# Optimization experiments

Hardware: AMD Instinct MI355X
Metric: run time of the kernel (lower is better)

Reference implementation:

```python
import math
import jax, jax.numpy as jnp
import numpy as np

# dims: layers, batch, seq, hidden, heads, ffn-mult
L, B, S, D, H, FFN = 2, 4, 2048, 256, 8, 4
HD = D // H          # head dim (= head v dim, double_v_dim=False)
EPS = 1e-5
SCALE_BASE = 512


def _ln(x, w, b):
    mu = x.mean(-1, keepdims=True)
    var = x.var(-1, keepdims=True)
    return (x - mu) * jax.lax.rsqrt(var + EPS) * w + b


def _xpos_tables():
    half = HD // 2
    sv = (np.arange(0, HD, 2) + 0.4 * HD) / (1.4 * HD)            # [half]
    pos = np.arange(S, dtype=np.float64)
    scale = sv[None, :] ** (pos[:, None] / SCALE_BASE)            # [S, half]
    inv_freq = 1.0 / (10000.0 ** (np.arange(half) / half))
    ang = pos[:, None] * inv_freq[None, :]                        # [S, half]
    return (jnp.asarray(np.sin(ang), jnp.float32),
            jnp.asarray(np.cos(ang), jnp.float32),
            jnp.asarray(scale, jnp.float32))

SIN, COS, XSCALE = _xpos_tables()


def _xpos(x, downscale=False):
    # x: [B, H, S, HD]
    sc = 1.0 / XSCALE if downscale else XSCALE
    sin2 = jnp.repeat(SIN * sc, 2, axis=-1)                       # [S, HD]
    cos2 = jnp.repeat(COS * sc, 2, axis=-1)
    x1, x2 = x[..., 0::2], x[..., 1::2]
    xr = jnp.stack((-x2, x1), axis=-1).reshape(x.shape)           # rotate_every_two
    return x * cos2 + xr * sin2


def _decay_mask():
    g = 1.0 - jnp.exp(jnp.linspace(math.log(1 / 32), math.log(1 / 512), H))
    n = jnp.arange(S)[:, None]
    m = jnp.arange(S)[None, :]
    keep = n >= m
    expo = jnp.where(keep, n - m, 0).astype(jnp.float32)
    return jnp.where(keep, g[:, None, None] ** expo[None], 0.0)   # [H, S, S]

DMASK = _decay_mask()


def setup_inputs() -> dict:
    key = jax.random.key(0)
    ks = jax.random.split(key, 16)
    sc = 1.0 / D
    f32 = jnp.float32
    return {
        "X":     jax.random.normal(ks[0], (B, S, D), f32),
        "Wq":    jax.random.normal(ks[1], (L, D, D), f32) * sc,
        "Wk":    jax.random.normal(ks[2], (L, D, D), f32) * sc,
        "Wv":    jax.random.normal(ks[3], (L, D, D), f32) * sc,
        "Wg":    jax.random.normal(ks[4], (L, D, D), f32) * sc,
        "Wo":    jax.random.normal(ks[5], (L, D, D), f32) * sc,
        "gn_w":  jnp.ones((L, D), f32) + 0.02 * jax.random.normal(ks[6], (L, D), f32),
        "gn_b":  0.02 * jax.random.normal(ks[7], (L, D), f32),
        "ln1_w": jnp.ones((L, D), f32),
        "ln1_b": jnp.zeros((L, D), f32),
        "ln2_w": jnp.ones((L, D), f32),
        "ln2_b": jnp.zeros((L, D), f32),
        "w1":    jax.random.normal(ks[8], (L, D, FFN * D), f32) * 0.02,
        "b1":    0.02 * jax.random.normal(ks[9], (L, FFN * D), f32),
        "w2":    jax.random.normal(ks[10], (L, FFN * D, D), f32) * 0.02,
        "b2":    0.02 * jax.random.normal(ks[11], (L, D), f32),
        "lnf_w": jnp.ones((D,), f32),
        "lnf_b": jnp.zeros((D,), f32),
    }


def reference(X, Wq, Wk, Wv, Wg, Wo, gn_w, gn_b, ln1_w, ln1_b,
              ln2_w, ln2_b, w1, b1, w2, b2, lnf_w, lnf_b):
    x = X
    for i in range(L):
        xn = _ln(x, ln1_w[i], ln1_b[i])                           # [B,S,D]
        q = (xn @ Wq[i]).reshape(B, S, H, HD).transpose(0, 2, 1, 3)
        k = (xn @ Wk[i]).reshape(B, S, H, HD).transpose(0, 2, 1, 3)
        v = (xn @ Wv[i]).reshape(B, S, H, HD).transpose(0, 2, 1, 3)
        q = _xpos(q)
        k = _xpos(k, downscale=True)
        att = jnp.einsum('bhnd,bhmd->bhnm', q, k) * DMASK          # [B,H,S,S]
        y = jnp.einsum('bhnm,bhmd->bhnd', att, v)                  # [B,H,S,HD]
        # GroupNorm(heads, v_dim): per-(b, position, head) normalization
        mu = y.mean(-1, keepdims=True)
        var = y.var(-1, keepdims=True)
        y = (y - mu) * jax.lax.rsqrt(var + EPS)
        y = y.transpose(0, 2, 1, 3).reshape(B, S, D)               # concat heads
        y = y * gn_w[i] + gn_b[i]
        g = xn @ Wg[i]
        ret = (g * jax.nn.sigmoid(g) * y) @ Wo[i]                  # swish gate + out proj
        yres = ret + x
        yn = _ln(yres, ln2_w[i], ln2_b[i])
        f = jax.nn.gelu(yn @ w1[i] + b1[i], approximate=False) @ w2[i] + b2[i]
        x = _ln(f + yres, lnf_w, lnf_b)
    return x
```

## Files before the change

kernel.cpp:

```cpp
#include <hip/hip_runtime.h>
#include <hip/hip_bf16.h>

typedef __hip_bfloat16 bf16;
typedef unsigned short ushort_t;
typedef __attribute__((ext_vector_type(8))) short short8v;
typedef __attribute__((ext_vector_type(4))) float f32x4;
typedef __attribute__((ext_vector_type(4))) unsigned int uint4v;

#define LYR 2
#define BB 4
#define SS 2048
#define DD 256
#define HH 8
#define HDD 32
#define FFD 1024
#define MM (BB*SS)

__device__ __forceinline__ unsigned int cvtpk(float lo, float hi) {
  unsigned int r;
  asm("v_cvt_pk_bf16_f32 %0, %1, %2" : "=v"(r) : "v"(lo), "v"(hi));
  return r;
}
__device__ __forceinline__ ushort_t f2b1(float x) { return (ushort_t)cvtpk(x, x); }

__device__ __forceinline__ void gload_lds16(const void* g, void* l) {
  __builtin_amdgcn_global_load_lds((const __attribute__((address_space(1))) void*)g,
                                   (__attribute__((address_space(3))) void*)l, 16, 0, 0);
}

__device__ __forceinline__ float l2g_of(int h) {
  return log2f(1.0f - expf(-3.4657359028f - 0.3960841187f * (float)h));
}

struct WDesc { const float* src; bf16* dst; int K; int N; };
struct WDescA { WDesc d[14]; float* tsn; float* tcs; float* tsc; };
__global__ __launch_bounds__(256) void wconv_k(WDescA da) {
  if (blockIdx.z == 14) {
    int i = (blockIdx.y * 32 + blockIdx.x) * 256 + threadIdx.y * 32 + threadIdx.x;
    if (i >= SS * 16) return;
    int s = i >> 4, j = i & 15;
    float sv = (2.0f * (float)j + 0.4f * (float)HDD) / (1.4f * (float)HDD);
    da.tsc[i] = powf(sv, (float)s * (1.0f / 512.0f));
    float inv_freq = powf(10000.0f, -(float)j * (1.0f / 16.0f));
    float ang = (float)s * inv_freq;
    da.tsn[i] = sinf(ang);
    da.tcs[i] = cosf(ang);
    return;
  }
  WDesc dd = da.d[blockIdx.z];
  int n0 = blockIdx.x * 32, k0 = blockIdx.y * 32;
  if (n0 >= dd.N || k0 >= dd.K) return;
  __shared__ float t[32][33];
  int tx = threadIdx.x, ty = threadIdx.y;
  #pragma unroll
  for (int i = 0; i < 32; i += 8) t[ty + i][tx] = dd.src[(size_t)(k0 + ty + i) * dd.N + n0 + tx];
  __syncthreads();
  #pragma unroll
  for (int i = 0; i < 32; i += 8) dd.dst[(size_t)(n0 + ty + i) * dd.K + k0 + tx] = __float2bfloat16(t[tx][ty + i]);
}

template<typename OT>
__global__ __launch_bounds__(256) void ln_k(const float* __restrict__ in, const float* __restrict__ w,
    const float* __restrict__ b, OT* __restrict__ out)
{
  int row = blockIdx.x, t = threadIdx.x;
  float v = in[(size_t)row * DD + t];
  __shared__ float red[4];
  float s = v;
  #pragma unroll
  for (int m = 32; m >= 1; m >>= 1) s += __shfl_xor(s, m);
  if ((t & 63) == 0) red[t >> 6] = s;
  __syncthreads();
  float mu = (red[0] + red[1] + red[2] + red[3]) * (1.0f / 256.0f);
  float d = v - mu;
  float s2 = d * d;
  #pragma unroll
  for (int m = 32; m >= 1; m >>= 1) s2 += __shfl_xor(s2, m);
  __syncthreads();
  if ((t & 63) == 0) red[t >> 6] = s2;
  __syncthreads();
  float var = (red[0] + red[1] + red[2] + red[3]) * (1.0f / 256.0f);
  float o = d * rsqrtf(var + 1e-5f) * w[t] + b[t];
  if constexpr (sizeof(OT) == 2) out[(size_t)row * DD + t] = __float2bfloat16(o);
  else                           out[(size_t)row * DD + t] = o;
}

#define STAGEG(buf, k0s) { \
    _Pragma("unroll") \
    for (int i = 0; i < BM / 32; ++i) { \
      int slot = i * 256 + tid; int row = slot >> 3, blk = slot & 7; \
      gload_lds16(Au + (size_t)(bm + row) * K + (k0s) + ((blk ^ (row & 7))) * 8, &Al[buf][slot * 8]); \
    } \
    _Pragma("unroll") \
    for (int i = 0; i < BN / 32; ++i) { \
      int slot = i * 256 + tid; int row = slot >> 3, blk = slot & 7; \
      gload_lds16(Bu + (size_t)(bn + row) * K + (k0s) + ((blk ^ (row & 7))) * 8, &Bl[buf][slot * 8]); \
    } }

enum { E_QKVG = 0 };

template<int BM, int BN, int K, int EPI>
__global__ __launch_bounds__(256) void mgemm_k(const bf16* __restrict__ Ag, const bf16* __restrict__ Wt,
    void* o0, void* o1, void* o2, void* o3,
    const float* __restrict__ tsn, const float* __restrict__ tcs, const float* __restrict__ tsc)
{
  constexpr int MT = BM / 32, NT = BN / 32;
  constexpr int WMH = BM / 2, WNH = BN / 2;
  __shared__ __align__(16) ushort_t Al[2][BM * 64];
  __shared__ __align__(16) ushort_t Bl[2][BN * 64];
  const int bm = blockIdx.x * BM;
  const int bn = blockIdx.y * BN;
  const int tid = threadIdx.x;
  const int lane = tid & 63, w = tid >> 6;
  const int lg = lane >> 4, ln = lane & 15;
  const int wr = w >> 1, wc = w & 1;
  const ushort_t* Au = (const ushort_t*)Ag;
  const ushort_t* Bu = (const ushort_t*)Wt;
  f32x4 acc[MT][NT] = {};

  STAGEG(0, 0)
  asm volatile("s_waitcnt vmcnt(0)" ::: "memory");
  __builtin_amdgcn_s_barrier();

  int cur = 0;
  for (int k0 = 0; k0 < K; k0 += 64) {
    if (k0 + 64 < K) STAGEG(cur ^ 1, k0 + 64)
    #pragma unroll
    for (int kh = 0; kh < 2; ++kh) {
      short8v af[MT], bfr[NT];
      #pragma unroll
      for (int mt = 0; mt < MT; ++mt) {
        int row = wr * WMH + mt * 16 + ln;
        af[mt] = *(const short8v*)&Al[cur][row * 64 + (((kh * 4 + lg) ^ (row & 7))) * 8];
      }
      #pragma unroll
      for (int nt = 0; nt < NT; ++nt) {
        int row = wc * WNH + nt * 16 + ln;
        bfr[nt] = *(const short8v*)&Bl[cur][row * 64 + (((kh * 4 + lg) ^ (row & 7))) * 8];
      }
      #pragma unroll
      for (int mt = 0; mt < MT; ++mt)
        #pragma unroll
        for (int nt = 0; nt < NT; ++nt)
          acc[mt][nt] = __builtin_amdgcn_mfma_f32_16x16x32_bf16(af[mt], bfr[nt], acc[mt][nt], 0, 0, 0);
    }
    asm volatile("s_waitcnt vmcnt(0)" ::: "memory");
    __builtin_amdgcn_s_barrier();
    cur ^= 1;
  }

  #pragma unroll
  for (int mt = 0; mt < MT; ++mt)
    #pragma unroll
    for (int nt = 0; nt < NT; ++nt) {
      const int colbase = bn + wc * WNH + nt * 16;
      const int sec = colbase >> 8;
      const int c = (colbase & 255) + ln;
      const int grow0 = bm + wr * WMH + mt * 16 + lg * 4;
      if (sec <= 1) {
        const int jj = (c & 31) >> 1;
        const float l2g = l2g_of(c >> 5);
        #pragma unroll
        for (int r = 0; r < 4; ++r) {
          const int grow = grow0 + r;
          const int s = grow & (SS - 1);
          float v = acc[mt][nt][r];
          float pv = __shfl_xor(v, 1);
          float scv = tsc[s * 16 + jj];
          if (sec == 1) scv = 1.0f / scv;
          float ce = tcs[s * 16 + jj] * scv, se = tsn[s * 16 + jj] * scv;
          float o = (ln & 1) ? (v * ce + pv * se) : (v * ce - pv * se);
          if (sec == 0) o *= exp2f(l2g * (float)s);
          bf16* dst = (sec == 0) ? (bf16*)o0 : (bf16*)o1;
          dst[(size_t)grow * DD + c] = __float2bfloat16(o);
        }
      } else if (sec == 2) {
        const int b = grow0 >> 11, s0 = grow0 & (SS - 1);
        const int h = c >> 5, d = c & 31;
        const float nl2g = -l2g_of(h);
        float v0 = acc[mt][nt][0] * exp2f(nl2g * (float)(s0 + 0));
        float v1 = acc[mt][nt][1] * exp2f(nl2g * (float)(s0 + 1));
        float v2 = acc[mt][nt][2] * exp2f(nl2g * (float)(s0 + 2));
        float v3 = acc[mt][nt][3] * exp2f(nl2g * (float)(s0 + 3));
        uint2 pk;
        pk.x = cvtpk(v0, v1);
        pk.y = cvtpk(v2, v3);
        *(uint2*)((ushort_t*)o2 + ((size_t)(b * 8 + h) * 32 + d) * SS + s0) = pk;
      } else {
        #pragma unroll
        for (int r = 0; r < 4; ++r)
          ((float*)o3)[(size_t)(grow0 + r) * DD + c] = acc[mt][nt][r];
      }
    }
}

template<bool LAST>
__global__ __launch_bounds__(256) void ffn_mega(
    const bf16* __restrict__ ubg, const bf16* __restrict__ wotg,
    const bf16* __restrict__ w1tg, const bf16* __restrict__ w2tg,
    const float* __restrict__ b1v, const float* __restrict__ b2v,
    const float* __restrict__ resin,
    float* __restrict__ yres, bf16* __restrict__ xn, float* __restrict__ dout,
    const float* __restrict__ l2w, const float* __restrict__ l2b,
    const float* __restrict__ lfw, const float* __restrict__ lfb,
    const float* __restrict__ l1w, const float* __restrict__ l1b)
{
  __shared__ __align__(16) ushort_t Bs[2][256 * 64];
  __shared__ __align__(16) ushort_t AX[4096];
  __shared__ __align__(16) ushort_t Us[4096];

  const int bm = blockIdx.x * 16;
  const int tid = threadIdx.x;
  const int lane = tid & 63, w = tid >> 6;
  const int lg = lane >> 4, ln = lane & 15;
  const int row0 = lg * 4;
  const ushort_t* ubu  = (const ushort_t*)ubg;
  const ushort_t* wotu = (const ushort_t*)wotg;
  const ushort_t* w1tu = (const ushort_t*)w1tg;
  const ushort_t* w2tu = (const ushort_t*)w2tg;
  float* red = (float*)Us;

  float resv[4][4];
  #pragma unroll
  for (int nt = 0; nt < 4; ++nt) {
    const int gcol = w * 64 + nt * 16 + ln;
    #pragma unroll
    for (int r = 0; r < 4; ++r)
      resv[nt][r] = resin[(size_t)(bm + row0 + r) * DD + gcol];
  }

  #define STAGEB(buf, base, stride, koff) { \
    _Pragma("unroll") \
    for (int i = 0; i < 8; ++i) { \
      int slot = i * 256 + tid; int row = slot >> 3, blk = slot & 7; \
      gload_lds16((base) + (size_t)row * (stride) + (koff) + ((blk ^ (row & 7))) * 8, &Bs[buf][slot * 8]); \
    } }
  #define STAGEA(buf, koff) { \
    if (tid < 128) { int row = tid >> 3, blk = tid & 7; \
      gload_lds16(ubu + (size_t)(bm + row) * DD + (koff) + ((blk ^ (row & 7))) * 8, &AX[(buf) * 1024 + tid * 8]); } }
  #define DRAIN asm volatile("s_waitcnt vmcnt(0)" ::: "memory"); __builtin_amdgcn_s_barrier();

  STAGEA(0, 0)
  STAGEB(0, wotu, 256, 0)
  DRAIN
  int cur = 0;

  f32x4 accw[4] = {};
  #pragma unroll
  for (int s = 0; s < 4; ++s) {
    if (s < 3) { STAGEA(cur ^ 1, (s + 1) * 64) STAGEB(cur ^ 1, wotu, 256, (s + 1) * 64) }
    else       { STAGEB(cur ^ 1, w1tu, 256, 0) }
    #pragma unroll
    for (int kh = 0; kh < 2; ++kh) {
      short8v af = *(const short8v*)&AX[cur * 1024 + ln * 64 + (((kh * 4 + lg) ^ (ln & 7))) * 8];
      #pragma unroll
      for (int nt = 0; nt < 4; ++nt) {
        int row = w * 64 + nt * 16 + ln;
        short8v bf_ = *(const short8v*)&Bs[cur][row * 64 + (((kh * 4 + lg) ^ (row & 7))) * 8];
        accw[nt] = __builtin_amdgcn_mfma_f32_16x16x32_bf16(af, bf_, accw[nt], 0, 0, 0);
      }
    }
    DRAIN
    cur ^= 1;
  }

  float v[4][4];
  #pragma unroll
  for (int nt = 0; nt < 4; ++nt)
    #pragma unroll
    for (int r = 0; r < 4; ++r) v[nt][r] = accw[nt][r] + resv[nt][r];
  float mu[4], rsg[4];
  {
    #pragma unroll
    for (int r = 0; r < 4; ++r) {
      float s1 = 0.f, s2 = 0.f;
      #pragma unroll
      for (int nt = 0; nt < 4; ++nt) { s1 += v[nt][r]; s2 += v[nt][r] * v[nt][r]; }
      #pragma unroll
      for (int m = 8; m >= 1; m >>= 1) { s1 += __shfl_xor(s1, m); s2 += __shfl_xor(s2, m); }
      if (ln == 0) { red[(w * 16 + row0 + r) * 2] = s1; red[(w * 16 + row0 + r) * 2 + 1] = s2; }
    }
    __syncthreads();
    #pragma unroll
    for (int r = 0; r < 4; ++r) {
      float S = 0.f, S2 = 0.f;
      #pragma unroll
      for (int ww = 0; ww < 4; ++ww) { S += red[(ww * 16 + row0 + r) * 2]; S2 += red[(ww * 16 + row0 + r) * 2 + 1]; }
      float m_ = S * (1.0f / 256.0f);
      mu[r] = m_; rsg[r] = rsqrtf(S2 * (1.0f / 256.0f) - m_ * m_ + 1e-5f);
    }
  }
  __syncthreads();
  #pragma unroll
  for (int nt = 0; nt < 4; ++nt) {
    const int gcol = w * 64 + nt * 16 + ln;
    const float lwv = l2w[gcol], lbv = l2b[gcol];
    const int off = nt * 16 + ln, blk = off >> 3, sub = off & 7;
    #pragma unroll
    for (int r = 0; r < 4; ++r) {
      const int row = row0 + r;
      float xv = (v[nt][r] - mu[r]) * rsg[r] * lwv + lbv;
      AX[row * 256 + w * 64 + ((blk ^ (row & 7)) << 3) + sub] = f2b1(xv);
    }
  }
  __syncthreads();

  f32x4 acc2[4] = {};
  #pragma unroll
  for (int c = 0; c < 4; ++c) {
    f32x4 acc1[4] = {};
    #pragma unroll
    for (int s = 0; s < 4; ++s) {
      if (s < 3) { STAGEB(cur ^ 1, w1tu + (size_t)c * 65536, 256, (s + 1) * 64) }
      else       { STAGEB(cur ^ 1, w2tu + c * 256, 1024, 0) }
      #pragma unroll
      for (int kh = 0; kh < 2; ++kh) {
        short8v af = *(const short8v*)&AX[ln * 256 + s * 64 + (((kh * 4 + lg) ^ (ln & 7))) * 8];
        #pragma unroll
        for (int nt = 0; nt < 4; ++nt) {
          int row = w * 64 + nt * 16 + ln;
          short8v bf_ = *(const short8v*)&Bs[cur][row * 64 + (((kh * 4 + lg) ^ (row & 7))) * 8];
          acc1[nt] = __builtin_amdgcn_mfma_f32_16x16x32_bf16(af, bf_, acc1[nt], 0, 0, 0);
        }
      }
      DRAIN
      cur ^= 1;
    }
    #pragma unroll
    for (int nt = 0; nt < 4; ++nt) {
      const int gcol1 = c * 256 + w * 64 + nt * 16 + ln;
      const float bb = b1v[gcol1];
      const int off = nt * 16 + ln, blk = off >> 3, sub = off & 7;
      #pragma unroll
      for (int r = 0; r < 4; ++r) {
        const int row = row0 + r;
        float t = acc1[nt][r] + bb;
        t = 0.5f * t * (1.0f + erff(t * 0.70710678118654752f));
        Us[row * 256 + w * 64 + ((blk ^ (row & 7)) << 3) + sub] = f2b1(t);
      }
    }
    __syncthreads();
    #pragma unroll
    for (int s = 0; s < 4; ++s) {
      if (s < 3)      { STAGEB(cur ^ 1, w2tu + c * 256, 1024, (s + 1) * 64) }
      else if (c < 3) { STAGEB(cur ^ 1, w1tu + (size_t)(c + 1) * 65536, 256, 0) }
      #pragma unroll
      for (int kh = 0; kh < 2; ++kh) {
        short8v af = *(const short8v*)&Us[ln * 256 + s * 64 + (((kh * 4 + lg) ^ (ln & 7))) * 8];
        #pragma unroll
        for (int nt = 0; nt < 4; ++nt) {
          int row = w * 64 + nt * 16 + ln;
          short8v bf_ = *(const short8v*)&Bs[cur][row * 64 + (((kh * 4 + lg) ^ (row & 7))) * 8];
          acc2[nt] = __builtin_amdgcn_mfma_f32_16x16x32_bf16(af, bf_, acc2[nt], 0, 0, 0);
        }
      }
      DRAIN
      cur ^= 1;
    }
  }

  float f[4][4];
  #pragma unroll
  for (int nt = 0; nt < 4; ++nt) {
    const int gcol = w * 64 + nt * 16 + ln;
    const float bb = b2v[gcol];
    #pragma unroll
    for (int r = 0; r < 4; ++r) f[nt][r] = acc2[nt][r] + bb + v[nt][r];
  }
  {
    #pragma unroll
    for (int r = 0; r < 4; ++r) {
      float s1 = 0.f, s2 = 0.f;
      #pragma unroll
      for (int nt = 0; nt < 4; ++nt) { s1 += f[nt][r]; s2 += f[nt][r] * f[nt][r]; }
      #pragma unroll
      for (int m = 8; m >= 1; m >>= 1) { s1 += __shfl_xor(s1, m); s2 += __shfl_xor(s2, m); }
      if (ln == 0) { red[(w * 16 + row0 + r) * 2] = s1; red[(w * 16 + row0 + r) * 2 + 1] = s2; }
    }
    __syncthreads();
    #pragma unroll
    for (int r = 0; r < 4; ++r) {
      float S = 0.f, S2 = 0.f;
      #pragma unroll
      for (int ww = 0; ww < 4; ++ww) { S += red[(ww * 16 + row0 + r) * 2]; S2 += red[(ww * 16 + row0 + r) * 2 + 1]; }
      float m_ = S * (1.0f / 256.0f);
      mu[r] = m_; rsg[r] = rsqrtf(S2 * (1.0f / 256.0f) - m_ * m_ + 1e-5f);
    }
  }
  float u[4][4];
  #pragma unroll
  for (int nt = 0; nt < 4; ++nt) {
    const int gcol = w * 64 + nt * 16 + ln;
    const float lwv = lfw[gcol], lbv = lfb[gcol];
    #pragma unroll
    for (int r = 0; r < 4; ++r)
      u[nt][r] = (f[nt][r] - mu[r]) * rsg[r] * lwv + lbv;
  }
  if constexpr (LAST) {
    #pragma unroll
    for (int nt = 0; nt < 4; ++nt) {
      const int gcol = w * 64 + nt * 16 + ln;
      #pragma unroll
      for (int r = 0; r < 4; ++r)
        dout[(size_t)(bm + row0 + r) * DD + gcol] = u[nt][r];
    }
  } else {
    __syncthreads();
    #pragma unroll
    for (int r = 0; r < 4; ++r) {
      float s1 = 0.f, s2 = 0.f;
      #pragma unroll
      for (int nt = 0; nt < 4; ++nt) { s1 += u[nt][r]; s2 += u[nt][r] * u[nt][r]; }
      #pragma unroll
      for (int m = 8; m >= 1; m >>= 1) { s1 += __shfl_xor(s1, m); s2 += __shfl_xor(s2, m); }
      if (ln == 0) { red[(w * 16 + row0 + r) * 2] = s1; red[(w * 16 + row0 + r) * 2 + 1] = s2; }
    }
    __syncthreads();
    float mu2[4], rs2[4];
    #pragma unroll
    for (int r = 0; r < 4; ++r) {
      float S = 0.f, S2 = 0.f;
      #pragma unroll
      for (int ww = 0; ww < 4; ++ww) { S += red[(ww * 16 + row0 + r) * 2]; S2 += red[(ww * 16 + row0 + r) * 2 + 1]; }
      float m_ = S * (1.0f / 256.0f);
      mu2[r] = m_; rs2[r] = rsqrtf(S2 * (1.0f / 256.0f) - m_ * m_ + 1e-5f);
    }
    #pragma unroll
    for (int nt = 0; nt < 4; ++nt) {
      const int gcol = w * 64 + nt * 16 + ln;
      const float lwv = l1w[gcol], lbv = l1b[gcol];
      #pragma unroll
      for (int r = 0; r < 4; ++r) {
        const size_t idx = (size_t)(bm + row0 + r) * DD + gcol;
        yres[idx] = u[nt][r];
        xn[idx] = __float2bfloat16((u[nt][r] - mu2[r]) * rs2[r] * lwv + lbv);
      }
    }
  }
  #undef STAGEB
  #undef STAGEA
  #undef DRAIN
}

__global__ __launch_bounds__(256) void attn_k(const bf16* __restrict__ qg, const bf16* __restrict__ kg,
    const bf16* __restrict__ vtg, const float* __restrict__ gbuf,
    const float* __restrict__ gnw, const float* __restrict__ gnb, bf16* __restrict__ ub)
{
  __shared__ __align__(16) ushort_t Kl[2][64 * 32];
  __shared__ __align__(16) ushort_t Vl[2][32 * 64];
  __shared__ __align__(16) unsigned int Pl[4][512];

  const int bh = blockIdx.x;
  const int b = bh >> 3, h = bh & (HH - 1);
  const int n0 = ((int)gridDim.y - 1 - (int)blockIdx.y) * 64;
  const int tid = threadIdx.x;
  const int w = tid >> 6, lane = tid & 63;
  const int lg = lane >> 4, ln = lane & 15;

  const size_t base = (size_t)b * SS * DD + h * HDD;
  const ushort_t* qp = (const ushort_t*)qg + base;
  const ushort_t* kp = (const ushort_t*)kg + base;
  const ushort_t* vtp = (const ushort_t*)vtg + (size_t)(b * 8 + h) * 32 * SS;

  const int n = n0 + w * 16 + ln;
  const short8v qf = *(const short8v*)(qp + (size_t)n * DD + lg * 8);

  const float l2g = l2g_of(h);
  f32x4 acc0 = {0,0,0,0}, acc1 = {0,0,0,0};

  const int Wwin = (int)(20.0f / (-l2g)) + 1;
  int m_lo = 0;
  if (n0 > Wwin) m_lo = ((n0 - Wwin) >> 6) << 6;

  const int Krow = tid >> 2, Kc8 = tid & 3;
  const int Vrow = tid >> 3, Vc8 = tid & 7;

  #define STAGE(buf, m0s) { \
    gload_lds16(kp + (size_t)((m0s) + Krow) * DD + ((Kc8 ^ (Krow & 3)) * 8), &Kl[buf][tid * 8]); \
    gload_lds16(vtp + (size_t)Vrow * SS + (m0s) + ((Vc8 ^ (Vrow & 7)) * 8), &Vl[buf][tid * 8]); }

  STAGE(0, m_lo)
  asm volatile("s_waitcnt vmcnt(0)" ::: "memory");
  __builtin_amdgcn_s_barrier();

  int cur = 0;
  for (int m0 = m_lo; m0 <= n0; m0 += 64) {
    if (m0 < n0) STAGE(cur ^ 1, m0 + 64)
    const bool diag = (m0 == n0);
    __builtin_amdgcn_s_setprio(1);
    #pragma unroll
    for (int mt = 0; mt < 4; ++mt) {
      const int krow = mt * 16 + ln;
      short8v kf = *(const short8v*)&Kl[cur][krow * 32 + ((lg ^ (krow & 3)) << 3)];
      f32x4 z = {0,0,0,0};
      f32x4 pa = __builtin_amdgcn_mfma_f32_16x16x32_bf16(kf, qf, z, 0, 0, 0);
      float v0 = pa[0], v1 = pa[1], v2 = pa[2], v3 = pa[3];
      if (diag) {
        const int m = n0 + mt * 16 + lg * 4;
        v0 = (n < m)     ? 0.f : v0;
        v1 = (n < m + 1) ? 0.f : v1;
        v2 = (n < m + 2) ? 0.f : v2;
        v3 = (n < m + 3) ? 0.f : v3;
      }
      uint2 pk;
      pk.x = cvtpk(v0, v1);
      pk.y = cvtpk(v2, v3);
      const int blk = (mt * 2 + (lg >> 1)) ^ (ln & 7);
      *(uint2*)&Pl[w][ln * 32 + blk * 4 + (lg & 1) * 2] = pk;
    }
    #pragma unroll
    for (int hh = 0; hh < 2; ++hh) {
      const int pblk = (hh * 4 + lg) ^ (ln & 7);
      uint4v pw = *(const uint4v*)&Pl[w][ln * 32 + pblk * 4];
      short8v pf = __builtin_bit_cast(short8v, pw);
      #pragma unroll
      for (int dt = 0; dt < 2; ++dt) {
        const int d = dt * 16 + ln;
        short8v vf = *(const short8v*)&Vl[cur][d * 64 + (((hh * 4 + lg) ^ (d & 7)) << 3)];
        if (dt == 0) acc0 = __builtin_amdgcn_mfma_f32_16x16x32_bf16(vf, pf, acc0, 0, 0, 0);
        else         acc1 = __builtin_amdgcn_mfma_f32_16x16x32_bf16(vf, pf, acc1, 0, 0, 0);
      }
    }
    __builtin_amdgcn_s_setprio(0);
    asm volatile("s_waitcnt vmcnt(0)" ::: "memory");
    __builtin_amdgcn_s_barrier();
    cur ^= 1;
  }
  #undef STAGE

  float gwv[8], gbv[8];
  #pragma unroll
  for (int dt = 0; dt < 2; ++dt) {
    f32x4 a = *(const f32x4*)&gnw[h * 32 + dt * 16 + lg * 4];
    f32x4 c = *(const f32x4*)&gnb[h * 32 + dt * 16 + lg * 4];
    #pragma unroll
    for (int r = 0; r < 4; ++r) { gwv[dt * 4 + r] = a[r]; gbv[dt * 4 + r] = c[r]; }
  }
  float s = 0.f;
  #pragma unroll
  for (int r = 0; r < 4; ++r) s += acc0[r] + acc1[r];
  s += __shfl_xor(s, 16); s += __shfl_xor(s, 32);
  const float mu = s * (1.0f / 32.0f);
  float s2 = 0.f;
  #pragma unroll
  for (int r = 0; r < 4; ++r) { float d0 = acc0[r] - mu, d1 = acc1[r] - mu; s2 += d0 * d0 + d1 * d1; }
  s2 += __shfl_xor(s2, 16); s2 += __shfl_xor(s2, 32);
  const float rs = rsqrtf(s2 * (1.0f / 32.0f) + 1e-5f);
  const size_t rowoff = ((size_t)b * SS + n) * DD + h * 32;
  #pragma unroll
  for (int dt = 0; dt < 2; ++dt) {
    f32x4 yv = dt ? acc1 : acc0;
    f32x4 gv = *(const f32x4*)&gbuf[rowoff + dt * 16 + lg * 4];
    float o0, o1, o2, o3;
    {
      float yn0 = (yv[0] - mu) * rs * gwv[dt * 4 + 0] + gbv[dt * 4 + 0];
      float yn1 = (yv[1] - mu) * rs * gwv[dt * 4 + 1] + gbv[dt * 4 + 1];
      float yn2 = (yv[2] - mu) * rs * gwv[dt * 4 + 2] + gbv[dt * 4 + 2];
      float yn3 = (yv[3] - mu) * rs * gwv[dt * 4 + 3] + gbv[dt * 4 + 3];
      o0 = gv[0] / (1.0f + expf(-gv[0])) * yn0;
      o1 = gv[1] / (1.0f + expf(-gv[1])) * yn1;
      o2 = gv[2] / (1.0f + expf(-gv[2])) * yn2;
      o3 = gv[3] / (1.0f + expf(-gv[3])) * yn3;
    }
    uint2 pk;
    pk.x = cvtpk(o0, o1);
    pk.y = cvtpk(o2, o3);
    *(uint2*)((ushort_t*)ub + rowoff + dt * 16 + lg * 4) = pk;
  }
}

extern "C" void kernel_launch(void* const* d_in, const int* in_sizes, int n_in,
                              void* d_out, int out_size, void* d_ws, size_t ws_size,
                              hipStream_t stream)
{
  const float* X    = (const float*)d_in[0];
  const float* Wq   = (const float*)d_in[1];
  const float* Wk   = (const float*)d_in[2];
  const float* Wv   = (const float*)d_in[3];
  const float* Wg   = (const float*)d_in[4];
  const float* Wo   = (const float*)d_in[5];
  const float* gnw  = (const float*)d_in[6];
  const float* gnb  = (const float*)d_in[7];
  const float* ln1w = (const float*)d_in[8];
  const float* ln1b = (const float*)d_in[9];
  const float* ln2w = (const float*)d_in[10];
  const float* ln2b = (const float*)d_in[11];
  const float* w1   = (const float*)d_in[12];
  const float* b1   = (const float*)d_in[13];
  const float* w2   = (const float*)d_in[14];
  const float* b2   = (const float*)d_in[15];
  const float* lnfw = (const float*)d_in[16];
  const float* lnfb = (const float*)d_in[17];

  char* p = (char*)d_ws;
  const size_t AF  = (size_t)MM * DD * sizeof(float);
  const size_t ABF = (size_t)MM * DD * sizeof(bf16);
  bf16*  xn   = (bf16*)p;  p += ABF;
  bf16*  qb   = (bf16*)p;  p += ABF;
  bf16*  kb   = (bf16*)p;  p += ABF;
  bf16*  vT   = (bf16*)p;  p += ABF;
  bf16*  ub   = (bf16*)p;  p += ABF;
  float* gbuf = (float*)p; p += AF;
  float* yres = (float*)p; p += AF;
  bf16*  wqkvgt = (bf16*)p; p += (size_t)2 * 1024 * 256 * sizeof(bf16);
  bf16*  wot    = (bf16*)p; p += (size_t)2 * 256 * 256 * sizeof(bf16);
  bf16*  w1t    = (bf16*)p; p += (size_t)2 * 1024 * 256 * sizeof(bf16);
  bf16*  w2t    = (bf16*)p; p += (size_t)2 * 256 * 1024 * sizeof(bf16);
  float* tsn  = (float*)p; p += SS * 16 * sizeof(float);
  float* tcs  = (float*)p; p += SS * 16 * sizeof(float);
  float* tsc  = (float*)p; p += SS * 16 * sizeof(float);

  {
    WDescA da;
    for (int l = 0; l < 2; ++l) {
      da.d[l * 7 + 0] = { Wq + (size_t)l * 65536, wqkvgt + (size_t)l * 262144 + 0 * 65536, 256, 256 };
      da.d[l * 7 + 1] = { Wk + (size_t)l * 65536, wqkvgt + (size_t)l * 262144 + 1 * 65536, 256, 256 };
      da.d[l * 7 + 2] = { Wv + (size_t)l * 65536, wqkvgt + (size_t)l * 262144 + 2 * 65536, 256, 256 };
      da.d[l * 7 + 3] = { Wg + (size_t)l * 65536, wqkvgt + (size_t)l * 262144 + 3 * 65536, 256, 256 };
      da.d[l * 7 + 4] = { Wo + (size_t)l * 65536, wot + (size_t)l * 65536, 256, 256 };
      da.d[l * 7 + 5] = { w1 + (size_t)l * 262144, w1t + (size_t)l * 262144, 256, 1024 };
      da.d[l * 7 + 6] = { w2 + (size_t)l * 262144, w2t + (size_t)l * 262144, 1024, 256 };
    }
    da.tsn = tsn; da.tcs = tcs; da.tsc = tsc;
    wconv_k<<<dim3(32, 32, 15), dim3(32, 8), 0, stream>>>(da);
  }

  ln_k<bf16><<<dim3(MM), 256, 0, stream>>>(X, ln1w, ln1b, xn);

  for (int l = 0; l < LYR; ++l) {
    mgemm_k<64, 128, DD, E_QKVG><<<dim3(MM / 64, 1024 / 128), 256, 0, stream>>>(
        xn, wqkvgt + (size_t)l * 262144, qb, kb, vT, gbuf, tsn, tcs, tsc);
    attn_k<<<dim3(BB * HH, SS / 64), 256, 0, stream>>>(qb, kb, vT, gbuf, gnw + l * DD, gnb + l * DD, ub);
    if (l == LYR - 1) {
      ffn_mega<true><<<dim3(MM / 16), 256, 0, stream>>>(
          ub, wot + (size_t)l * 65536, w1t + (size_t)l * 262144, w2t + (size_t)l * 262144,
          b1 + l * FFD, b2 + l * DD, (l == 0) ? X : yres,
          nullptr, nullptr, (float*)d_out,
          ln2w + l * DD, ln2b + l * DD, lnfw, lnfb, nullptr, nullptr);
    } else {
      ffn_mega<false><<<dim3(MM / 16), 256, 0, stream>>>(
          ub, wot + (size_t)l * 65536, w1t + (size_t)l * 262144, w2t + (size_t)l * 262144,
          b1 + l * FFD, b2 + l * DD, (l == 0) ? X : yres,
          yres, xn, nullptr,
          ln2w + l * DD, ln2b + l * DD, lnfw, lnfb, ln1w + (l + 1) * DD, ln1b + (l + 1) * DD);
    }
  }
}
```

Before: 200.6 us.

## Give each wave a private weight tile in ffn_mega and drop block barriers

The FFN megakernel's shared double-buffered weight tile becomes four single-buffered per-wave tiles, so each wave loads only the 64 weight rows it consumes. Block-wide barriers inside the W1/W2 K-loops become per-wave vmcnt waits, and launch bounds request three blocks per CU now that LDS use is smaller. The cost is that the weight prefetch that overlapped the MFMA work is gone: each wave now loads, waits, then computes, and relies on other waves or blocks to hide memory latency. With 512 blocks over 256 CUs, the extra occupancy may not be used.

```diff
diff --git a/kernel.cpp b/kernel.cpp
--- a/kernel.cpp
+++ b/kernel.cpp
@@ -195,7 +195,7 @@
 }
 
 template<bool LAST>
-__global__ __launch_bounds__(256) void ffn_mega(
+__global__ __launch_bounds__(256, 3) void ffn_mega(
     const bf16* __restrict__ ubg, const bf16* __restrict__ wotg,
     const bf16* __restrict__ w1tg, const bf16* __restrict__ w2tg,
     const float* __restrict__ b1v, const float* __restrict__ b2v,
@@ -205,7 +205,7 @@
     const float* __restrict__ lfw, const float* __restrict__ lfb,
     const float* __restrict__ l1w, const float* __restrict__ l1b)
 {
-  __shared__ __align__(16) ushort_t Bs[2][256 * 64];
+  __shared__ __align__(16) ushort_t Bs[4][4096];
   __shared__ __align__(16) ushort_t AX[4096];
   __shared__ __align__(16) ushort_t Us[4096];
 
@@ -229,38 +229,39 @@
       resv[nt][r] = resin[(size_t)(bm + row0 + r) * DD + gcol];
   }
 
-  #define STAGEB(buf, base, stride, koff) { \
+  #define STAGEBW(base, stride, nbase, koff) { \
     _Pragma("unroll") \
     for (int i = 0; i < 8; ++i) { \
-      int slot = i * 256 + tid; int row = slot >> 3, blk = slot & 7; \
-      gload_lds16((base) + (size_t)row * (stride) + (koff) + ((blk ^ (row & 7))) * 8, &Bs[buf][slot * 8]); \
+      int slot = i * 64 + lane; int r = slot >> 3, blk = slot & 7; \
+      gload_lds16((base) + (size_t)((nbase) + w * 64 + r) * (stride) + (koff) + ((blk ^ (r & 7))) * 8, &Bs[w][slot * 8]); \
     } }
   #define STAGEA(buf, koff) { \
-    if (tid < 128) { int row = tid >> 3, blk = tid & 7; \
-      gload_lds16(ubu + (size_t)(bm + row) * DD + (koff) + ((blk ^ (row & 7))) * 8, &AX[(buf) * 1024 + tid * 8]); } }
-  #define DRAIN asm volatile("s_waitcnt vmcnt(0)" ::: "memory"); __builtin_amdgcn_s_barrier();
+    if (tid < 128) { int rr = tid >> 3, blk = tid & 7; \
+      gload_lds16(ubu + (size_t)(bm + rr) * DD + (koff) + ((blk ^ (rr & 7))) * 8, &AX[(buf) * 1024 + tid * 8]); } }
+  #define WAVEWAIT asm volatile("s_waitcnt vmcnt(0)" ::: "memory");
 
   STAGEA(0, 0)
-  STAGEB(0, wotu, 256, 0)
-  DRAIN
+  STAGEBW(wotu, 256, 0, 0)
+  WAVEWAIT
+  __builtin_amdgcn_s_barrier();
   int cur = 0;
-
   f32x4 accw[4] = {};
   #pragma unroll
   for (int s = 0; s < 4; ++s) {
-    if (s < 3) { STAGEA(cur ^ 1, (s + 1) * 64) STAGEB(cur ^ 1, wotu, 256, (s + 1) * 64) }
-    else       { STAGEB(cur ^ 1, w1tu, 256, 0) }
+    if (s < 3) STAGEA(cur ^ 1, (s + 1) * 64)
     #pragma unroll
     for (int kh = 0; kh < 2; ++kh) {
       short8v af = *(const short8v*)&AX[cur * 1024 + ln * 64 + (((kh * 4 + lg) ^ (ln & 7))) * 8];
       #pragma unroll
       for (int nt = 0; nt < 4; ++nt) {
-        int row = w * 64 + nt * 16 + ln;
-        short8v bf_ = *(const short8v*)&Bs[cur][row * 64 + (((kh * 4 + lg) ^ (row & 7))) * 8];
+        int r = nt * 16 + ln;
+        short8v bf_ = *(const short8v*)&Bs[w][r * 64 + (((kh * 4 + lg) ^ (r & 7))) * 8];
         accw[nt] = __builtin_amdgcn_mfma_f32_16x16x32_bf16(af, bf_, accw[nt], 0, 0, 0);
       }
     }
-    DRAIN
+    if (s < 3) STAGEBW(wotu, 256, 0, (s + 1) * 64)
+    WAVEWAIT
+    __builtin_amdgcn_s_barrier();
     cur ^= 1;
   }
 
@@ -290,7 +291,6 @@
       mu[r] = m_; rsg[r] = rsqrtf(S2 * (1.0f / 256.0f) - m_ * m_ + 1e-5f);
     }
   }
-  __syncthreads();
   #pragma unroll
   for (int nt = 0; nt < 4; ++nt) {
     const int gcol = w * 64 + nt * 16 + ln;
@@ -311,21 +311,20 @@
     f32x4 acc1[4] = {};
     #pragma unroll
     for (int s = 0; s < 4; ++s) {
-      if (s < 3) { STAGEB(cur ^ 1, w1tu + (size_t)c * 65536, 256, (s + 1) * 64) }
-      else       { STAGEB(cur ^ 1, w2tu + c * 256, 1024, 0) }
+      STAGEBW(w1tu, 256, c * 256, s * 64)
+      WAVEWAIT
       #pragma unroll
       for (int kh = 0; kh < 2; ++kh) {
         short8v af = *(const short8v*)&AX[ln * 256 + s * 64 + (((kh * 4 + lg) ^ (ln & 7))) * 8];
         #pragma unroll
         for (int nt = 0; nt < 4; ++nt) {
-          int row = w * 64 + nt * 16 + ln;
-          short8v bf_ = *(const short8v*)&Bs[cur][row * 64 + (((kh * 4 + lg) ^ (row & 7))) * 8];
+          int r = nt * 16 + ln;
+          short8v bf_ = *(const short8v*)&Bs[w][r * 64 + (((kh * 4 + lg) ^ (r & 7))) * 8];
           acc1[nt] = __builtin_amdgcn_mfma_f32_16x16x32_bf16(af, bf_, acc1[nt], 0, 0, 0);
         }
       }
-      DRAIN
-      cur ^= 1;
-    }
+    }
+    __syncthreads();
     #pragma unroll
     for (int nt = 0; nt < 4; ++nt) {
       const int gcol1 = c * 256 + w * 64 + nt * 16 + ln;
@@ -342,22 +341,21 @@
     __syncthreads();
     #pragma unroll
     for (int s = 0; s < 4; ++s) {
-      if (s < 3)      { STAGEB(cur ^ 1, w2tu + c * 256, 1024, (s + 1) * 64) }
-      else if (c < 3) { STAGEB(cur ^ 1, w1tu + (size_t)(c + 1) * 65536, 256, 0) }
+      STAGEBW(w2tu, 1024, 0, c * 256 + s * 64)
+      WAVEWAIT
       #pragma unroll
       for (int kh = 0; kh < 2; ++kh) {
         short8v af = *(const short8v*)&Us[ln * 256 + s * 64 + (((kh * 4 + lg) ^ (ln & 7))) * 8];
         #pragma unroll
         for (int nt = 0; nt < 4; ++nt) {
-          int row = w * 64 + nt * 16 + ln;
-          short8v bf_ = *(const short8v*)&Bs[cur][row * 64 + (((kh * 4 + lg) ^ (row & 7))) * 8];
+          int r = nt * 16 + ln;
+          short8v bf_ = *(const short8v*)&Bs[w][r * 64 + (((kh * 4 + lg) ^ (r & 7))) * 8];
           acc2[nt] = __builtin_amdgcn_mfma_f32_16x16x32_bf16(af, bf_, acc2[nt], 0, 0, 0);
         }
       }
-      DRAIN
-      cur ^= 1;
-    }
-  }
+    }
+  }
+  __syncthreads();
 
   float f[4][4];
   #pragma unroll
@@ -437,9 +435,9 @@
       }
     }
   }
-  #undef STAGEB
+  #undef STAGEBW
   #undef STAGEA
-  #undef DRAIN
+  #undef WAVEWAIT
 }
 
 __global__ __launch_bounds__(256) void attn_k(const bf16* __restrict__ qg, const bf16* __restrict__ kg,
```

Result: faster. 192.0 us (-4.3%).
